# Performance work log

Measured on AMD Instinct MI355X. Metric: run time of the kernel, lower is better.

The kernel has to match this reference:

```python
import jax, jax.numpy as jnp
import numpy as np

E = 1024      # embbed_size
NH = 64       # num_hiddens (per-head dim)
H = 16        # num_heads (NH*H == E)
B = 8192
S = 2
EPS = 1e-5


def setup_inputs() -> dict:
    key = jax.random.key(0)
    ks = jax.random.split(key, 20)
    g = lambda i, shape, scale: (jax.random.normal(ks[i], shape, dtype=jnp.float32) * scale)
    d = {
        "input": g(0, (B, S, E), 1.0),
        # attention projections (bias=False), torch Linear weight layout (out, in)
        "Wq": g(1, (NH * H, E), E ** -0.5),
        "Wk": g(2, (NH * H, E), E ** -0.5),
        "Wv": g(3, (NH * H, E), E ** -0.5),
        "Wo": g(4, (E, NH * H), E ** -0.5),
        # layernorms over [2, E]
        "ln1_w": jnp.ones((S, E), jnp.float32),
        "ln1_b": jnp.zeros((S, E), jnp.float32),
        "ln2_w": jnp.ones((S, E), jnp.float32),
        "ln2_b": jnp.zeros((S, E), jnp.float32),
        # ffn1 / ffn2: Linear(E,2E)+Tanh+Linear(2E,E)+Tanh (bias=True default)
        "f1w1": g(5, (2 * E, E), E ** -0.5), "f1b1": jnp.zeros((2 * E,), jnp.float32),
        "f1w2": g(6, (E, 2 * E), (2 * E) ** -0.5), "f1b2": jnp.zeros((E,), jnp.float32),
        "f2w1": g(7, (2 * E, E), E ** -0.5), "f2b1": jnp.zeros((2 * E,), jnp.float32),
        "f2w2": g(8, (E, 2 * E), (2 * E) ** -0.5), "f2b2": jnp.zeros((E,), jnp.float32),
    }
    return d


def _layernorm2d(x, w, b):
    # torch LayerNorm([2, E]): normalize jointly over the last TWO dims
    m = jnp.mean(x, axis=(-2, -1), keepdims=True)
    v = jnp.mean(jnp.square(x - m), axis=(-2, -1), keepdims=True)
    return (x - m) * jax.lax.rsqrt(v + EPS) * w + b


def _split_heads(x):
    # faithful to transpose_qkv: reshape(B,S,NH,H) then permute(0,3,1,2) -> (B,H,S,NH)
    return x.reshape(B, S, NH, H).transpose(0, 3, 1, 2)


def reference(input, Wq, Wk, Wv, Wo, ln1_w, ln1_b, ln2_w, ln2_b,
              f1w1, f1b1, f1w2, f1b2, f2w1, f2b1, f2w2, f2b2):
    xs = _layernorm2d(input, ln1_w, ln1_b)                 # (B,S,E)
    q = _split_heads(xs @ Wq.T)                            # (B,H,S,NH)
    k = _split_heads(xs @ Wk.T)
    v = _split_heads(xs @ Wv.T)
    att = jnp.einsum("bhsd,bhtd->bhst", q, k) / np.sqrt(NH)
    out = jnp.einsum("bhst,bhtd->bhsd", jax.nn.softmax(att, axis=-1), v)  # (B,H,S,NH)
    # permute(0,2,3,1) -> (B,S,NH,H), reshape -> (B,S,NH*H)
    concat = out.transpose(0, 2, 3, 1).reshape(B, S, NH * H)
    res = concat @ Wo.T                                    # (B,S,E)
    out1 = input + res
    out_s = _layernorm2d(out1, ln2_w, ln2_b)
    s0 = jnp.tanh(jnp.tanh(out_s[:, 0, :] @ f1w1.T + f1b1) @ f1w2.T + f1b2)
    s1 = jnp.tanh(jnp.tanh(out_s[:, 1, :] @ f2w1.T + f2b1) @ f2w2.T + f2b2)
    return jnp.stack((s0, s1), axis=1) + out1
```

## Files before the change

kernel.cpp:

```cpp
#include <hip/hip_runtime.h>
#include <hip/hip_bf16.h>
#include <stdint.h>


typedef __attribute__((ext_vector_type(8))) short short8;
typedef __attribute__((ext_vector_type(4))) float floatx4;

__device__ __forceinline__ float b2f(short s) {
  union { unsigned u; float f; } v;
  v.u = ((unsigned)(unsigned short)s) << 16;
  return v.f;
}
__device__ __forceinline__ short f2b(float f) {
  union { float f; unsigned u; } v;
  v.f = f;
  unsigned r = v.u + 0x7FFFu + ((v.u >> 16) & 1u);
  return (short)(r >> 16);
}
__device__ __forceinline__ float fast_tanh(float x) {
  float e = __expf(2.f * x);
  return 1.f - 2.f / (e + 1.f);
}
__device__ __forceinline__ void load16_lds(const void* g, void* l) {
  __builtin_amdgcn_global_load_lds(
      (__attribute__((address_space(1))) void*)(void*)g,
      (__attribute__((address_space(3))) void*)l, 16, 0, 0);
}

struct Src4 { const float* p[4]; };

__global__ __launch_bounds__(256) void cvt4_kernel(Src4 s,
                                                   short* __restrict__ y,
                                                   int sh) {
  const int i = blockIdx.x * 256 + threadIdx.x;
  const int seg = i >> sh;
  const int off = i & ((1 << sh) - 1);
  const float* x = s.p[seg];
  const float4 a = ((const float4*)x)[(size_t)off * 2];
  const float4 b = ((const float4*)x)[(size_t)off * 2 + 1];
  short8 r;
  r[0] = f2b(a.x); r[1] = f2b(a.y); r[2] = f2b(a.z); r[3] = f2b(a.w);
  r[4] = f2b(b.x); r[5] = f2b(b.y); r[6] = f2b(b.z); r[7] = f2b(b.w);
  ((short8*)y)[i] = r;
}

template <int EPI, int ZSEL>
__global__ __launch_bounds__(512, 2) void gemm256(
    const short* A, int lda, const short* W, int K, void* Cout, int ldc,
    const float* aux, int ld_aux, const float* bias, const short* res, int ldr,
    const short* Wz, const float* biasz, int a_zoff, int c_zoff) {
  extern __shared__ short lds[];
  const int tid = threadIdx.x;
  const int lane = tid & 63;
  const int wid = tid >> 6;
  const int l15 = lane & 15;
  const int l4 = lane >> 4;
  const int wm = (wid >> 2) * 128;
  const int wn = (wid & 3) * 64;

  const int gx = gridDim.x;
  const int nwg = gx * gridDim.y;
  const int bid0 = blockIdx.y * gx + blockIdx.x;
  const int bid = (bid0 & 7) * (nwg >> 3) + (bid0 >> 3);
  const int bn0 = (bid % gx) * 256;
  const int bm0 = (bid / gx) * 256;

  const short* Wp = W;
  const float* bp = bias;
  int coff = 0;
  if (ZSEL && blockIdx.z) {
    Wp = Wz;
    bp = biasz;
    A += a_zoff;
    coff = c_zoff;
  }

  floatx4 zero = {0.f, 0.f, 0.f, 0.f};
  floatx4 acc[8][4];
#pragma unroll
  for (int i = 0; i < 8; ++i)
#pragma unroll
    for (int j = 0; j < 4; ++j) acc[i][j] = zero;

  const int r8 = lane >> 3;
  const int gsw = (lane & 7) ^ r8;
  const int aoff = r8 * lda + gsw * 8;
  const int boff = r8 * K + gsw * 8;
  const short* Ab = A + (size_t)bm0 * lda;
  const short* Bb = Wp + (size_t)bn0 * K;
  const int e0 = __builtin_amdgcn_readfirstlane(wid * 4);
  const int swz = l15 & 7;

  short* As0 = lds;
  short* As1 = lds + 16384;
  short* Bs0 = lds + 32768;
  short* Bs1 = lds + 49152;

#define STAGE_A(slotptr, t, tk0) \
  load16_lds(Ab + (size_t)(e0 + (t)) * 8 * lda + (tk0) + aoff, \
             (slotptr) + (e0 + (t)) * 512)
#define STAGE_B(slotptr, t, tk0) \
  load16_lds(Bb + (size_t)(e0 + (t)) * 8 * K + (tk0) + boff, \
             (slotptr) + (e0 + (t)) * 512)

  short8 av[4], bv[4];

#define PHASE(Asl, Bsl, kk, mh, STAGE_STMT, DOWAIT)                          \
  {                                                                          \
    const int ko = (((kk)*4 + l4) ^ swz) * 8;                                \
    if ((mh) == 0) {                                                         \
      _Pragma("unroll") for (int j = 0; j < 4; ++j)                          \
          bv[j] = *(const short8*)&(Bsl)[(wn + j * 16 + l15) * 64 + ko];     \
    }                                                                        \
    _Pragma("unroll") for (int i = 0; i < 4; ++i)                            \
        av[i] = *(const short8*)&(Asl)[(wm + (mh)*64 + i * 16 + l15) * 64 +  \
                                       ko];                                  \
    STAGE_STMT;                                                              \
    asm volatile("" ::: "memory");                                           \
    __builtin_amdgcn_s_barrier();                                            \
    __builtin_amdgcn_s_setprio(1);                                           \
    _Pragma("unroll") for (int i = 0; i < 4; ++i)                            \
        _Pragma("unroll") for (int j = 0; j < 4; ++j)                        \
            acc[(mh)*4 + i][j] = __builtin_amdgcn_mfma_f32_16x16x32_bf16(    \
                av[i], bv[j], acc[(mh)*4 + i][j], 0, 0, 0);                  \
    __builtin_amdgcn_s_setprio(0);                                           \
    if (DOWAIT) asm volatile("s_waitcnt vmcnt(0)" ::: "memory");             \
    asm volatile("" ::: "memory");                                           \
    __builtin_amdgcn_s_barrier();                                            \
  }

#pragma unroll
  for (int t = 0; t < 4; ++t) {
    STAGE_A(As0, t, 0);
    STAGE_B(Bs0, t, 0);
  }
  asm volatile("s_waitcnt vmcnt(0)" ::: "memory");
  __builtin_amdgcn_s_barrier();

  const int nit = K >> 7;
  for (int it = 0; it < nit; ++it) {
    const int kodd = it * 128 + 64;
    const int knext = it * 128 + 128;
    const bool more = (it + 1 < nit);
    PHASE(As0, Bs0, 0, 0, { STAGE_A(As1, 0, kodd); STAGE_B(Bs1, 0, kodd); }, 0)
    PHASE(As0, Bs0, 0, 1, { STAGE_A(As1, 1, kodd); STAGE_B(Bs1, 1, kodd); }, 0)
    PHASE(As0, Bs0, 1, 0, { STAGE_A(As1, 2, kodd); STAGE_B(Bs1, 2, kodd); }, 0)
    PHASE(As0, Bs0, 1, 1, { STAGE_A(As1, 3, kodd); STAGE_B(Bs1, 3, kodd); }, 1)
    PHASE(As1, Bs1, 0, 0,
          { if (more) { STAGE_A(As0, 0, knext); STAGE_B(Bs0, 0, knext); } }, 0)
    PHASE(As1, Bs1, 0, 1,
          { if (more) { STAGE_A(As0, 1, knext); STAGE_B(Bs0, 1, knext); } }, 0)
    PHASE(As1, Bs1, 1, 0,
          { if (more) { STAGE_A(As0, 2, knext); STAGE_B(Bs0, 2, knext); } }, 0)
    PHASE(As1, Bs1, 1, 1,
          { if (more) { STAGE_A(As0, 3, knext); STAGE_B(Bs0, 3, knext); } }, 1)
  }
#undef PHASE
#undef STAGE_A
#undef STAGE_B

  const int mb = bm0 + wm + l4 * 4;
  const int nb = bn0 + wn + l15;
#pragma unroll
  for (int i = 0; i < 8; ++i) {
#pragma unroll
    for (int p = 0; p < 4; ++p) {
      const int r = mb + i * 16 + p;
#pragma unroll
      for (int j = 0; j < 4; ++j) {
        const int n = nb + j * 16;
        float c = acc[i][j][p];
        if (EPI == 0) {
          ((short*)Cout)[(size_t)r * ldc + n + coff] = f2b(c);
        } else if (EPI == 1) {
          ((short*)Cout)[(size_t)r * ldc + n + coff] =
              f2b(c + aux[(size_t)r * ld_aux + n]);
        } else if (EPI == 2) {
          ((short*)Cout)[(size_t)r * ldc + n + coff] =
              f2b(fast_tanh(c + bp[n]));
        } else {
          const float rv = b2f(res[(size_t)r * ldr + n + coff]);
          ((float*)Cout)[(size_t)r * ldc + n + coff] =
              fast_tanh(c + bp[n]) + rv;
        }
      }
    }
  }
}

template <int INBF16>
__global__ __launch_bounds__(256) void ln_kernel(const void* __restrict__ xin,
                                                 const float* __restrict__ w,
                                                 const float* __restrict__ bb,
                                                 short* __restrict__ y) {
  const int b = blockIdx.x;
  const int tid = threadIdx.x;
  const size_t base = (size_t)b * 2048 + tid * 8;
  float xv[8];
  if (INBF16) {
    short8 s = *(const short8*)((const short*)xin + base);
#pragma unroll
    for (int j = 0; j < 8; ++j) xv[j] = b2f(s[j]);
  } else {
    const float4 a = *(const float4*)((const float*)xin + base);
    const float4 c = *(const float4*)((const float*)xin + base + 4);
    xv[0] = a.x; xv[1] = a.y; xv[2] = a.z; xv[3] = a.w;
    xv[4] = c.x; xv[5] = c.y; xv[6] = c.z; xv[7] = c.w;
  }
  float sum = 0.f, sq = 0.f;
#pragma unroll
  for (int j = 0; j < 8; ++j) {
    sum += xv[j];
    sq += xv[j] * xv[j];
  }
  __shared__ float rs[8];
  const int lane = tid & 63, wid = tid >> 6;
#pragma unroll
  for (int off = 32; off; off >>= 1) {
    sum += __shfl_down(sum, off);
    sq += __shfl_down(sq, off);
  }
  if (lane == 0) {
    rs[wid] = sum;
    rs[4 + wid] = sq;
  }
  __syncthreads();
  const float stot = rs[0] + rs[1] + rs[2] + rs[3];
  const float qtot = rs[4] + rs[5] + rs[6] + rs[7];
  const float mean = stot * (1.f / 2048.f);
  const float rstd = rsqrtf(qtot * (1.f / 2048.f) - mean * mean + 1e-5f);
  const int wi = tid * 8;
  short8 r;
#pragma unroll
  for (int j = 0; j < 8; ++j)
    r[j] = f2b((xv[j] - mean) * rstd * w[wi + j] + bb[wi + j]);
  *(short8*)(y + base) = r;
}

__global__ __launch_bounds__(256) void attn_kernel(short* qkv) {
  __shared__ short sm[2][6][1032];
  __shared__ float sps[2][2][2][16];
  __shared__ float spp[2][2][2][16];
  const int tid = threadIdx.x;
  const int half = tid >> 7;
  const int t = tid & 127;
  const int b = blockIdx.x * 2 + half;
  const short* row0 = qkv + ((size_t)b * 2 + 0) * 3072;
  const short* row1 = qkv + ((size_t)b * 2 + 1) * 3072;
  const short* srcs[6] = {row0,        row1,        row0 + 1024,
                          row1 + 1024, row0 + 2048, row1 + 2048};
#pragma unroll
  for (int rr = 0; rr < 6; ++rr)
    *(short8*)&sm[half][rr][t * 8] = *(const short8*)(srcs[rr] + t * 8);
  __syncthreads();
  if (t < 64) {
    const int h = t & 15, comb = t >> 4;
    const int si = comb >> 1, ti = comb & 1;
    const short* qr = sm[half][si];
    const short* kr = sm[half][2 + ti];
    float a = 0.f;
#pragma unroll
    for (int d = 0; d < 64; ++d) a += b2f(qr[d * 16 + h]) * b2f(kr[d * 16 + h]);
    sps[half][si][ti][h] = a * 0.125f;
  }
  __syncthreads();
  if (t < 32) {
    const int h = t & 15, si = t >> 4;
    const float s0 = sps[half][si][0][h], s1 = sps[half][si][1][h];
    const float m = fmaxf(s0, s1);
    const float e0 = __expf(s0 - m), e1 = __expf(s1 - m);
    const float inv = 1.f / (e0 + e1);
    spp[half][si][0][h] = e0 * inv;
    spp[half][si][1][h] = e1 * inv;
  }
  __syncthreads();
#pragma unroll
  for (int si = 0; si < 2; ++si) {
    short8 r;
#pragma unroll
    for (int j = 0; j < 8; ++j) {
      const int e = t * 8 + j;
      const int h = e & 15;
      const float c = spp[half][si][0][h] * b2f(sm[half][4][e]) +
                      spp[half][si][1][h] * b2f(sm[half][5][e]);
      r[j] = f2b(c);
    }
    *(short8*)(qkv + ((size_t)b * 2 + si) * 3072 + t * 8) = r;
  }
}

extern "C" void kernel_launch(void* const* d_in, const int* in_sizes, int n_in,
                              void* d_out, int out_size, void* d_ws,
                              size_t ws_size, hipStream_t stream) {
  (void)in_sizes; (void)n_in; (void)out_size; (void)ws_size;
  const float* input = (const float*)d_in[0];
  const float* Wq = (const float*)d_in[1];
  const float* Wk = (const float*)d_in[2];
  const float* Wv = (const float*)d_in[3];
  const float* Wo = (const float*)d_in[4];
  const float* ln1w = (const float*)d_in[5];
  const float* ln1b = (const float*)d_in[6];
  const float* ln2w = (const float*)d_in[7];
  const float* ln2b = (const float*)d_in[8];
  const float* f1w1 = (const float*)d_in[9];
  const float* f1b1 = (const float*)d_in[10];
  const float* f1w2 = (const float*)d_in[11];
  const float* f1b2 = (const float*)d_in[12];
  const float* f2w1 = (const float*)d_in[13];
  const float* f2b1 = (const float*)d_in[14];
  const float* f2w2 = (const float*)d_in[15];
  const float* f2b2 = (const float*)d_in[16];
  float* out = (float*)d_out;
  char* ws = (char*)d_ws;

  const size_t MB = 1024 * 1024;
  dim3 blk(256);
  dim3 gblk(512);
  const int GLDS = 131072;

  {
    auto set = [](const void* f) {
      (void)hipFuncSetAttribute(f, hipFuncAttributeMaxDynamicSharedMemorySize,
                                131072);
    };
    set((const void*)gemm256<0, 0>);
    set((const void*)gemm256<1, 0>);
    set((const void*)gemm256<2, 1>);
    set((const void*)gemm256<3, 1>);
  }

  short* wqkv = (short*)ws;
  short* wo = (short*)(ws + 6 * MB);
  short* xs = (short*)(ws + 8 * MB);
  short* out1 = xs;
  short* qkvb = (short*)(ws + 40 * MB);

  {
    Src4 s{{Wq, Wk, Wv, Wo}};
    cvt4_kernel<<<2048, blk, 0, stream>>>(s, wqkv, 17);
  }
  ln_kernel<0><<<8192, blk, 0, stream>>>(input, ln1w, ln1b, xs);
  {
    dim3 g(12, 64);
    gemm256<0, 0><<<g, gblk, GLDS, stream>>>(xs, 1024, wqkv, 1024, qkvb, 3072,
                                             nullptr, 0, nullptr, nullptr, 0,
                                             nullptr, nullptr, 0, 0);
  }
  attn_kernel<<<4096, blk, 0, stream>>>(qkvb);
  {
    dim3 g(4, 64);
    gemm256<1, 0><<<g, gblk, GLDS, stream>>>(qkvb, 3072, wo, 1024, out1, 1024,
                                             input, 1024, nullptr, nullptr, 0,
                                             nullptr, nullptr, 0, 0);
  }

  short* fw1s0 = (short*)(ws + 40 * MB);
  short* fw1s1 = (short*)(ws + 44 * MB);
  short* fw2s0 = (short*)(ws + 48 * MB);
  short* fw2s1 = (short*)(ws + 52 * MB);
  short* hb = (short*)(ws + 56 * MB);
  short* outs = (short*)out;
  {
    Src4 s{{f1w1, f2w1, f1w2, f2w2}};
    cvt4_kernel<<<4096, blk, 0, stream>>>(s, fw1s0, 18);
  }
  ln_kernel<1><<<8192, blk, 0, stream>>>(out1, ln2w, ln2b, outs);
  {
    dim3 g1(8, 32, 2);
    gemm256<2, 1><<<g1, gblk, GLDS, stream>>>(
        outs, 2048, fw1s0, 1024, hb, 4096, nullptr, 0, f1b1, nullptr, 0,
        fw1s1, f2b1, 1024, 2048);
    dim3 g2(4, 32, 2);
    gemm256<3, 1><<<g2, gblk, GLDS, stream>>>(
        hb, 4096, fw2s0, 2048, out, 2048, nullptr, 0, f1b2, out1, 2048,
        fw2s1, f2b2, 2048, 1024);
  }
}
```

Measured before the change: 525.7 us.

## Restructure GEMM main loop to one barrier per K tile

Replaces the eight-phase GEMM inner loop, which had a barrier around each phase, with a per-tile body. Each K tile now issues all of the next tile's global-to-LDS loads up front, then reads LDS fragments and runs the MFMAs in interleaved groups. It finishes with a single waitcnt and barrier. The goal is to cut barrier stalls and let LDS reads overlap with MFMA work, at the cost of more live registers for the fragments and less interleaving of staging loads across phases.

New measurement: 538.0 us. 1.02x slower.

```diff
diff --git a/kernel.cpp b/kernel.cpp
--- a/kernel.cpp
+++ b/kernel.cpp
@@ -103,30 +103,56 @@
   load16_lds(Bb + (size_t)(e0 + (t)) * 8 * K + (tk0) + boff, \
              (slotptr) + (e0 + (t)) * 512)
 
-  short8 av[4], bv[4];
-
-#define PHASE(Asl, Bsl, kk, mh, STAGE_STMT, DOWAIT)                          \
+#define TILE(Asl, Bsl, Anx, Bnx, knext, domore)                              \
   {                                                                          \
-    const int ko = (((kk)*4 + l4) ^ swz) * 8;                                \
-    if ((mh) == 0) {                                                         \
-      _Pragma("unroll") for (int j = 0; j < 4; ++j)                          \
-          bv[j] = *(const short8*)&(Bsl)[(wn + j * 16 + l15) * 64 + ko];     \
+    if (domore) {                                                            \
+      STAGE_A(Anx, 0, knext); STAGE_B(Bnx, 0, knext);                        \
+      STAGE_A(Anx, 1, knext); STAGE_B(Bnx, 1, knext);                        \
+      STAGE_A(Anx, 2, knext); STAGE_B(Bnx, 2, knext);                        \
+      STAGE_A(Anx, 3, knext); STAGE_B(Bnx, 3, knext);                        \
     }                                                                        \
-    _Pragma("unroll") for (int i = 0; i < 4; ++i)                            \
-        av[i] = *(const short8*)&(Asl)[(wm + (mh)*64 + i * 16 + l15) * 64 +  \
-                                       ko];                                  \
-    STAGE_STMT;                                                              \
-    asm volatile("" ::: "memory");                                           \
-    __builtin_amdgcn_s_barrier();                                            \
+    short8 bv0[4], bv1[4], a00[4], a01[4], a10[4], a11[4];                   \
+    const int ko0 = (l4 ^ swz) * 8;                                          \
+    const int ko1 = ((4 + l4) ^ swz) * 8;                                    \
+    _Pragma("unroll") for (int j = 0; j < 4; ++j)                            \
+        bv0[j] = *(const short8*)&(Bsl)[(wn + j * 16 + l15) * 64 + ko0];     \
+    _Pragma("unroll") for (int i = 0; i < 4; ++i)                            \
+        a00[i] = *(const short8*)&(Asl)[(wm + i * 16 + l15) * 64 + ko0];     \
+    _Pragma("unroll") for (int i = 0; i < 4; ++i)                            \
+        a01[i] = *(const short8*)&(Asl)[(wm + 64 + i * 16 + l15) * 64 + ko0];\
     __builtin_amdgcn_s_setprio(1);                                           \
     _Pragma("unroll") for (int i = 0; i < 4; ++i)                            \
         _Pragma("unroll") for (int j = 0; j < 4; ++j)                        \
-            acc[(mh)*4 + i][j] = __builtin_amdgcn_mfma_f32_16x16x32_bf16(    \
-                av[i], bv[j], acc[(mh)*4 + i][j], 0, 0, 0);                  \
+            acc[i][j] = __builtin_amdgcn_mfma_f32_16x16x32_bf16(             \
+                a00[i], bv0[j], acc[i][j], 0, 0, 0);                         \
     __builtin_amdgcn_s_setprio(0);                                           \
-    if (DOWAIT) asm volatile("s_waitcnt vmcnt(0)" ::: "memory");             \
-    asm volatile("" ::: "memory");                                           \
-    __builtin_amdgcn_s_barrier();                                            \
+    _Pragma("unroll") for (int j = 0; j < 4; ++j)                            \
+        bv1[j] = *(const short8*)&(Bsl)[(wn + j * 16 + l15) * 64 + ko1];     \
+    _Pragma("unroll") for (int i = 0; i < 4; ++i)                            \
+        a10[i] = *(const short8*)&(Asl)[(wm + i * 16 + l15) * 64 + ko1];     \
+    __builtin_amdgcn_s_setprio(1);                                           \
+    _Pragma("unroll") for (int i = 0; i < 4; ++i)                            \
+        _Pragma("unroll") for (int j = 0; j < 4; ++j)                        \
+            acc[4 + i][j] = __builtin_amdgcn_mfma_f32_16x16x32_bf16(         \
+                a01[i], bv0[j], acc[4 + i][j], 0, 0, 0);                     \
+    __builtin_amdgcn_s_setprio(0);                                           \
+    _Pragma("unroll") for (int i = 0; i < 4; ++i)                            \
+        a11[i] = *(const short8*)&(Asl)[(wm + 64 + i * 16 + l15) * 64 + ko1];\
+    __builtin_amdgcn_s_setprio(1);                                           \
+    _Pragma("unroll") for (int i = 0; i < 4; ++i)                            \
+        _Pragma("unroll") for (int j = 0; j < 4; ++j)                        \
+            acc[i][j] = __builtin_amdgcn_mfma_f32_16x16x32_bf16(             \
+                a10[i], bv1[j], acc[i][j], 0, 0, 0);                         \
+    _Pragma("unroll") for (int i = 0; i < 4; ++i)                            \
+        _Pragma("unroll") for (int j = 0; j < 4; ++j)                        \
+            acc[4 + i][j] = __builtin_amdgcn_mfma_f32_16x16x32_bf16(         \
+                a11[i], bv1[j], acc[4 + i][j], 0, 0, 0);                     \
+    __builtin_amdgcn_s_setprio(0);                                           \
+    if (domore) {                                                            \
+      asm volatile("s_waitcnt vmcnt(0)" ::: "memory");                       \
+      __builtin_amdgcn_s_barrier();                                          \
+      asm volatile("" ::: "memory");                                         \
+    }                                                                        \
   }
 
 #pragma unroll
@@ -136,26 +162,17 @@
   }
   asm volatile("s_waitcnt vmcnt(0)" ::: "memory");
   __builtin_amdgcn_s_barrier();
+  asm volatile("" ::: "memory");
 
   const int nit = K >> 7;
   for (int it = 0; it < nit; ++it) {
     const int kodd = it * 128 + 64;
     const int knext = it * 128 + 128;
     const bool more = (it + 1 < nit);
-    PHASE(As0, Bs0, 0, 0, { STAGE_A(As1, 0, kodd); STAGE_B(Bs1, 0, kodd); }, 0)
-    PHASE(As0, Bs0, 0, 1, { STAGE_A(As1, 1, kodd); STAGE_B(Bs1, 1, kodd); }, 0)
-    PHASE(As0, Bs0, 1, 0, { STAGE_A(As1, 2, kodd); STAGE_B(Bs1, 2, kodd); }, 0)
-    PHASE(As0, Bs0, 1, 1, { STAGE_A(As1, 3, kodd); STAGE_B(Bs1, 3, kodd); }, 1)
-    PHASE(As1, Bs1, 0, 0,
-          { if (more) { STAGE_A(As0, 0, knext); STAGE_B(Bs0, 0, knext); } }, 0)
-    PHASE(As1, Bs1, 0, 1,
-          { if (more) { STAGE_A(As0, 1, knext); STAGE_B(Bs0, 1, knext); } }, 0)
-    PHASE(As1, Bs1, 1, 0,
-          { if (more) { STAGE_A(As0, 2, knext); STAGE_B(Bs0, 2, knext); } }, 0)
-    PHASE(As1, Bs1, 1, 1,
-          { if (more) { STAGE_A(As0, 3, knext); STAGE_B(Bs0, 3, knext); } }, 1)
-  }
-#undef PHASE
+    TILE(As0, Bs0, As1, Bs1, kodd, true)
+    TILE(As1, Bs1, As0, Bs0, knext, more)
+  }
+#undef TILE
 #undef STAGE_A
 #undef STAGE_B
 
```

## Restructure GEMM mainloop into 4-slot K=32 pipeline with three stages in flight

Applied to the files above, without the earlier changes.

Replaces the two-buffer K=64 staging scheme with a four-slot ring of K=32 tiles, keeping three tiles of global-to-LDS loads in flight and waiting with partial vmcnt counts instead of draining to zero. The LDS tile row width shrinks to 32 elements with a new XOR swizzle, and B fragments are loaded once per slot. The intent is to hide global memory latency better and avoid full vmcnt(0) stalls. The cost is more barriers per unit of K, more loop iterations, and reliance on exact vmcnt accounting for correctness.

Result: faster. 511.3 us (-2.8%).

```diff
diff --git a/kernel.cpp b/kernel.cpp
--- a/kernel.cpp
+++ b/kernel.cpp
@@ -82,82 +82,78 @@
 #pragma unroll
     for (int j = 0; j < 4; ++j) acc[i][j] = zero;
 
-  const int r8 = lane >> 3;
-  const int gsw = (lane & 7) ^ r8;
-  const int aoff = r8 * lda + gsw * 8;
-  const int boff = r8 * K + gsw * 8;
+  const int r16 = lane >> 2;
+  const int srcg = (lane & 3) ^ ((lane >> 3) & 3);
+  const int aoff = r16 * lda + srcg * 8;
+  const int boff = r16 * K + srcg * 8;
   const short* Ab = A + (size_t)bm0 * lda;
   const short* Bb = Wp + (size_t)bn0 * K;
-  const int e0 = __builtin_amdgcn_readfirstlane(wid * 4);
-  const int swz = l15 & 7;
-
-  short* As0 = lds;
-  short* As1 = lds + 16384;
-  short* Bs0 = lds + 32768;
-  short* Bs1 = lds + 49152;
-
-#define STAGE_A(slotptr, t, tk0) \
-  load16_lds(Ab + (size_t)(e0 + (t)) * 8 * lda + (tk0) + aoff, \
-             (slotptr) + (e0 + (t)) * 512)
-#define STAGE_B(slotptr, t, tk0) \
-  load16_lds(Bb + (size_t)(e0 + (t)) * 8 * K + (tk0) + boff, \
-             (slotptr) + (e0 + (t)) * 512)
-
-  short8 av[4], bv[4];
-
-#define PHASE(Asl, Bsl, kk, mh, STAGE_STMT, DOWAIT)                          \
+  const int e0 = __builtin_amdgcn_readfirstlane(wid * 2);
+  const int ko = ((l4 ^ ((l15 >> 1) & 3)) * 8);
+
+#define STAGE_A32(p, t, kb) \
+  load16_lds(Ab + (size_t)(e0 + (t)) * 16 * lda + (kb) + aoff, \
+             lds + (p) * 8192 + (e0 + (t)) * 512)
+#define STAGE_B32(p, t, kb) \
+  load16_lds(Bb + (size_t)(e0 + (t)) * 16 * K + (kb) + boff, \
+             lds + 32768 + (p) * 8192 + (e0 + (t)) * 512)
+
+#define SLOT32(sp, np, kb, DOSTAGE, WAITSTMT)                                \
   {                                                                          \
-    const int ko = (((kk)*4 + l4) ^ swz) * 8;                                \
-    if ((mh) == 0) {                                                         \
-      _Pragma("unroll") for (int j = 0; j < 4; ++j)                          \
-          bv[j] = *(const short8*)&(Bsl)[(wn + j * 16 + l15) * 64 + ko];     \
-    }                                                                        \
+    const short* Ap = lds + (sp) * 8192;                                     \
+    const short* Bp = lds + 32768 + (sp) * 8192;                             \
+    short8 av[4], bv[4];                                                     \
+    if (DOSTAGE) { STAGE_A32(np, 0, kb); STAGE_A32(np, 1, kb); }             \
+    _Pragma("unroll") for (int j = 0; j < 4; ++j)                            \
+        bv[j] = *(const short8*)&Bp[(wn + j * 16 + l15) * 32 + ko];          \
     _Pragma("unroll") for (int i = 0; i < 4; ++i)                            \
-        av[i] = *(const short8*)&(Asl)[(wm + (mh)*64 + i * 16 + l15) * 64 +  \
-                                       ko];                                  \
-    STAGE_STMT;                                                              \
+        av[i] = *(const short8*)&Ap[(wm + i * 16 + l15) * 32 + ko];          \
     asm volatile("" ::: "memory");                                           \
     __builtin_amdgcn_s_barrier();                                            \
     __builtin_amdgcn_s_setprio(1);                                           \
     _Pragma("unroll") for (int i = 0; i < 4; ++i)                            \
         _Pragma("unroll") for (int j = 0; j < 4; ++j)                        \
-            acc[(mh)*4 + i][j] = __builtin_amdgcn_mfma_f32_16x16x32_bf16(    \
-                av[i], bv[j], acc[(mh)*4 + i][j], 0, 0, 0);                  \
+            acc[i][j] = __builtin_amdgcn_mfma_f32_16x16x32_bf16(             \
+                av[i], bv[j], acc[i][j], 0, 0, 0);                           \
     __builtin_amdgcn_s_setprio(0);                                           \
-    if (DOWAIT) asm volatile("s_waitcnt vmcnt(0)" ::: "memory");             \
     asm volatile("" ::: "memory");                                           \
     __builtin_amdgcn_s_barrier();                                            \
-  }
-
-#pragma unroll
-  for (int t = 0; t < 4; ++t) {
-    STAGE_A(As0, t, 0);
-    STAGE_B(Bs0, t, 0);
-  }
-  asm volatile("s_waitcnt vmcnt(0)" ::: "memory");
+    if (DOSTAGE) { STAGE_B32(np, 0, kb); STAGE_B32(np, 1, kb); }             \
+    _Pragma("unroll") for (int i = 0; i < 4; ++i)                            \
+        av[i] = *(const short8*)&Ap[(wm + 64 + i * 16 + l15) * 32 + ko];     \
+    asm volatile("" ::: "memory");                                           \
+    __builtin_amdgcn_s_barrier();                                            \
+    __builtin_amdgcn_s_setprio(1);                                           \
+    _Pragma("unroll") for (int i = 0; i < 4; ++i)                            \
+        _Pragma("unroll") for (int j = 0; j < 4; ++j)                        \
+            acc[4 + i][j] = __builtin_amdgcn_mfma_f32_16x16x32_bf16(         \
+                av[i], bv[j], acc[4 + i][j], 0, 0, 0);                       \
+    __builtin_amdgcn_s_setprio(0);                                           \
+    WAITSTMT;                                                                \
+    asm volatile("" ::: "memory");                                           \
+    __builtin_amdgcn_s_barrier();                                            \
+  }
+
+#pragma unroll
+  for (int t = 0; t < 2; ++t) { STAGE_A32(0, t, 0);  STAGE_B32(0, t, 0); }
+#pragma unroll
+  for (int t = 0; t < 2; ++t) { STAGE_A32(1, t, 32); STAGE_B32(1, t, 32); }
+#pragma unroll
+  for (int t = 0; t < 2; ++t) { STAGE_A32(2, t, 64); STAGE_B32(2, t, 64); }
+  asm volatile("s_waitcnt vmcnt(8)" ::: "memory");
   __builtin_amdgcn_s_barrier();
 
-  const int nit = K >> 7;
-  for (int it = 0; it < nit; ++it) {
-    const int kodd = it * 128 + 64;
-    const int knext = it * 128 + 128;
-    const bool more = (it + 1 < nit);
-    PHASE(As0, Bs0, 0, 0, { STAGE_A(As1, 0, kodd); STAGE_B(Bs1, 0, kodd); }, 0)
-    PHASE(As0, Bs0, 0, 1, { STAGE_A(As1, 1, kodd); STAGE_B(Bs1, 1, kodd); }, 0)
-    PHASE(As0, Bs0, 1, 0, { STAGE_A(As1, 2, kodd); STAGE_B(Bs1, 2, kodd); }, 0)
-    PHASE(As0, Bs0, 1, 1, { STAGE_A(As1, 3, kodd); STAGE_B(Bs1, 3, kodd); }, 1)
-    PHASE(As1, Bs1, 0, 0,
-          { if (more) { STAGE_A(As0, 0, knext); STAGE_B(Bs0, 0, knext); } }, 0)
-    PHASE(As1, Bs1, 0, 1,
-          { if (more) { STAGE_A(As0, 1, knext); STAGE_B(Bs0, 1, knext); } }, 0)
-    PHASE(As1, Bs1, 1, 0,
-          { if (more) { STAGE_A(As0, 2, knext); STAGE_B(Bs0, 2, knext); } }, 0)
-    PHASE(As1, Bs1, 1, 1,
-          { if (more) { STAGE_A(As0, 3, knext); STAGE_B(Bs0, 3, knext); } }, 1)
-  }
-#undef PHASE
-#undef STAGE_A
-#undef STAGE_B
+  const int nk = K >> 5;
+  for (int s = 0; s + 3 < nk; ++s) {
+    SLOT32(s & 3, (s + 3) & 3, (s + 3) * 32, 1,
+           asm volatile("s_waitcnt vmcnt(8)" ::: "memory"))
+  }
+  SLOT32((nk - 3) & 3, 0, 0, 0, asm volatile("s_waitcnt vmcnt(4)" ::: "memory"))
+  SLOT32((nk - 2) & 3, 0, 0, 0, asm volatile("s_waitcnt vmcnt(0)" ::: "memory"))
+  SLOT32((nk - 1) & 3, 0, 0, 0, (void)0)
+#undef SLOT32
+#undef STAGE_A32
+#undef STAGE_B32
 
   const int mb = bm0 + wm + l4 * 4;
   const int nb = bn0 + wn + l15;
```
